# Optimization experiments

Hardware: AMD Instinct MI355X
Metric: run time of the kernel (lower is better)

The kernel has to match this reference:

```python
import jax, jax.numpy as jnp
import numpy as np

N_REAL = 1_000_000
C_IN = 32
C_OUT = 32
PAD = 1_050_000


def setup_inputs() -> dict:
    key = jax.random.key(0)
    k_x, k_fn, k_w0, k_w1, k_w2, k_b = jax.random.split(key, 6)
    x = jax.random.normal(k_x, (N_REAL, C_IN), dtype=jnp.float32)
    face_neighborhood = jax.random.randint(k_fn, (N_REAL, 9), 0, PAD, dtype=jnp.int32)
    # real faces occupy the first N_REAL padded slots; the rest are pads
    face_is_pad = jnp.arange(PAD) >= N_REAL
    # kaiming-uniform-style init for [out, in] weights (fan_in = C_IN for 1x1 taps)
    bw = 1.0 / np.sqrt(C_IN)
    w0 = jax.random.uniform(k_w0, (C_OUT, C_IN), jnp.float32, -bw, bw)
    w1 = jax.random.uniform(k_w1, (C_OUT, C_IN), jnp.float32, -bw, bw)
    w2 = jax.random.uniform(k_w2, (C_OUT, C_IN), jnp.float32, -bw, bw)
    bb = 1.0 / np.sqrt(C_IN * 9)  # fan_in of the full (out,in,1,9) kernel
    bias = jax.random.uniform(k_b, (C_OUT,), jnp.float32, -bb, bb)
    return {"x": x, "w0": w0, "w1": w1, "w2": w2, "bias": bias,
            "face_neighborhood": face_neighborhood, "face_is_pad": face_is_pad,
            "pad_size": PAD}


def reference(x, w0, w1, w2, bias, face_neighborhood, face_is_pad, pad_size):
    # Scatter x into padded buffer: padded_x[~face_is_pad] = x (jit-safe via cumsum map)
    keep = jnp.logical_not(face_is_pad)
    src = jnp.cumsum(keep.astype(jnp.int32)) - 1  # index into x for each kept slot
    padded_x = jnp.where(keep[:, None], x[jnp.clip(src, 0, x.shape[0] - 1)],
                         jnp.zeros((), x.dtype))  # [pad_size, C]
    # Symmetric 1x9 filter = [w0, w1, w2, w1, w2, w1, w2, w1, w2]:
    # fold the 9 gathers into 3 groups before the tiny GEMMs.
    g0 = padded_x[face_neighborhood[:, 0]]
    g1 = (padded_x[face_neighborhood[:, 1]] + padded_x[face_neighborhood[:, 3]]
          + padded_x[face_neighborhood[:, 5]] + padded_x[face_neighborhood[:, 7]])
    g2 = (padded_x[face_neighborhood[:, 2]] + padded_x[face_neighborhood[:, 4]]
          + padded_x[face_neighborhood[:, 6]] + padded_x[face_neighborhood[:, 8]])
    out = (jnp.einsum('nc,oc->no', g0, w0)
           + jnp.einsum('nc,oc->no', g1, w1)
           + jnp.einsum('nc,oc->no', g2, w2)
           + bias)
    return out
```

## Files before the change

### kernel.cpp

```cpp
#include <hip/hip_runtime.h>
#include <hip/hip_fp16.h>

typedef _Float16 half8 __attribute__((ext_vector_type(8)));
typedef _Float16 half4v __attribute__((ext_vector_type(4)));
typedef float float4v __attribute__((ext_vector_type(4)));
typedef int int4a __attribute__((ext_vector_type(4), aligned(4)));

#define BLOCK 256
#define ROWS_PER_BLOCK 64
#define ROWPITCH 104

__device__ _Float16 g_wh[6 * 512];

__global__ void prep_weights(const float* __restrict__ w0,
                             const float* __restrict__ w1,
                             const float* __restrict__ w2) {
    const int t = threadIdx.x;
    const int st = t >> 6;
    const int lane = t & 63;
    const int s = st >> 1, tt = st & 1;
    const float* w = (s == 0) ? w0 : (s == 1) ? w1 : w2;
    const int o = tt * 16 + (lane & 15);
    const int k = (lane >> 4) * 8;
    #pragma unroll
    for (int j = 0; j < 8; ++j)
        g_wh[st * 512 + lane * 8 + j] = (_Float16)w[o * 32 + k + j];
}

__global__ __launch_bounds__(256) void convert_x(const float* __restrict__ x,
                                                 _Float16* __restrict__ xh,
                                                 int n8) {
    const int stride = gridDim.x * 256;
    for (int i = blockIdx.x * 256 + threadIdx.x; i < n8; i += stride) {
        const float4v a = __builtin_nontemporal_load(reinterpret_cast<const float4v*>(x) + 2 * (long)i);
        const float4v b = __builtin_nontemporal_load(reinterpret_cast<const float4v*>(x) + 2 * (long)i + 1);
        half8 h = {(_Float16)a.x, (_Float16)a.y, (_Float16)a.z, (_Float16)a.w,
                   (_Float16)b.x, (_Float16)b.y, (_Float16)b.z, (_Float16)b.w};
        *(half8*)(xh + 8 * (long)i) = h;
    }
}

__global__ __launch_bounds__(BLOCK) void face_conv_f16(
    const _Float16* __restrict__ xh,
    const float* __restrict__ bias,
    const int* __restrict__ fn,
    float* __restrict__ out,
    int N)
{
    __shared__ alignas(16) _Float16 A[4][16 * ROWPITCH];

    const int tid  = threadIdx.x;
    const int wave = tid >> 6;
    const int lane = tid & 63;
    const int m16  = lane & 15;
    const int quad = lane >> 4;
    const int r    = lane >> 2;
    const int c8   = (lane & 3) * 8;

    half8 bfrag[3][2];
    #pragma unroll
    for (int s = 0; s < 3; ++s)
        #pragma unroll
        for (int t = 0; t < 2; ++t)
            bfrag[s][t] = *(const half8*)(g_wh + (s * 2 + t) * 512 + lane * 8);
    const float bias0 = bias[m16];
    const float bias1 = bias[16 + m16];

    const int base = blockIdx.x * ROWS_PER_BLOCK + wave * 16;
    _Float16* Aw = A[wave];

    int row = base + r;
    row = (row < N) ? row : (N - 1);
    const int* fr = fn + (long)row * 9;
    const int4a i03 = __builtin_nontemporal_load(reinterpret_cast<const int4a*>(fr));
    const int4a i47 = __builtin_nontemporal_load(reinterpret_cast<const int4a*>(fr + 4));
    const int  i8s  = __builtin_nontemporal_load(fr + 8);
    const int idx[9] = {i03.x, i03.y, i03.z, i03.w, i47.x, i47.y, i47.z, i47.w, i8s};

    half8 v[9];
    #pragma unroll
    for (int j = 0; j < 9; ++j) {
        const int id = idx[j];
        if ((unsigned)id < (unsigned)N) {
            v[j] = *(const half8*)(xh + (long)id * 32 + c8);
        } else {
            v[j] = (half8){0, 0, 0, 0, 0, 0, 0, 0};
        }
    }
    half8 g0 = v[0], g1, g2;
    #pragma unroll
    for (int e = 0; e < 8; ++e) {
        g1[e] = (_Float16)((float)v[1][e] + (float)v[3][e] + (float)v[5][e] + (float)v[7][e]);
        g2[e] = (_Float16)((float)v[2][e] + (float)v[4][e] + (float)v[6][e] + (float)v[8][e]);
    }
    _Float16* dst = Aw + r * ROWPITCH + c8;
    *(half8*)(dst)      = g0;
    *(half8*)(dst + 32) = g1;
    *(half8*)(dst + 64) = g2;

    __syncthreads();

    float4v acc0 = {0.f, 0.f, 0.f, 0.f}, acc1 = {0.f, 0.f, 0.f, 0.f};
    #pragma unroll
    for (int s = 0; s < 3; ++s) {
        half8 a = *(half8*)(Aw + m16 * ROWPITCH + s * 32 + quad * 8);
        acc0 = __builtin_amdgcn_mfma_f32_16x16x32_f16(a, bfrag[s][0], acc0, 0, 0, 0);
        acc1 = __builtin_amdgcn_mfma_f32_16x16x32_f16(a, bfrag[s][1], acc1, 0, 0, 0);
    }

    #pragma unroll
    for (int i = 0; i < 4; ++i) {
        const int rr = base + quad * 4 + i;
        if (rr < N) {
            __builtin_nontemporal_store(acc0[i] + bias0, &out[(long)rr * 32 + m16]);
            __builtin_nontemporal_store(acc1[i] + bias1, &out[(long)rr * 32 + 16 + m16]);
        }
    }
}

__global__ __launch_bounds__(BLOCK) void face_conv_kernel(
    const float* __restrict__ x,
    const float* __restrict__ bias,
    const int* __restrict__ fn,
    float* __restrict__ out,
    int N)
{
    __shared__ alignas(16) _Float16 A[4][16 * ROWPITCH];

    const int tid  = threadIdx.x;
    const int wave = tid >> 6;
    const int lane = tid & 63;
    const int m16  = lane & 15;
    const int quad = lane >> 4;
    const int oct  = lane >> 3;
    const int m8   = lane & 7;

    half8 bfrag[3][2];
    #pragma unroll
    for (int s = 0; s < 3; ++s)
        #pragma unroll
        for (int t = 0; t < 2; ++t)
            bfrag[s][t] = *(const half8*)(g_wh + (s * 2 + t) * 512 + lane * 8);
    const float bias0 = bias[m16];
    const float bias1 = bias[16 + m16];

    const int base = blockIdx.x * ROWS_PER_BLOCK + wave * 16;
    _Float16* Aw = A[wave];

    int idx[2][9];
    #pragma unroll
    for (int it = 0; it < 2; ++it) {
        int r = base + it * 8 + oct;
        r = (r < N) ? r : (N - 1);
        const int* fr = fn + (long)r * 9;
        #pragma unroll
        for (int j = 0; j < 9; ++j) idx[it][j] = __builtin_nontemporal_load(fr + j);
    }

    #pragma unroll
    for (int it = 0; it < 2; ++it) {
        float4v v[9];
        #pragma unroll
        for (int j = 0; j < 9; ++j) {
            const int id = idx[it][j];
            if ((unsigned)id < (unsigned)N) {
                v[j] = *(const float4v*)(x + (long)id * 32 + m8 * 4);
            } else {
                v[j] = (float4v){0.f, 0.f, 0.f, 0.f};
            }
        }
        const float4v g0 = v[0];
        const float4v g1 = v[1] + v[3] + v[5] + v[7];
        const float4v g2 = v[2] + v[4] + v[6] + v[8];
        _Float16* dst = Aw + (it * 8 + oct) * ROWPITCH + m8 * 4;
        *(half4v*)(dst)      = (half4v){(_Float16)g0.x, (_Float16)g0.y, (_Float16)g0.z, (_Float16)g0.w};
        *(half4v*)(dst + 32) = (half4v){(_Float16)g1.x, (_Float16)g1.y, (_Float16)g1.z, (_Float16)g1.w};
        *(half4v*)(dst + 64) = (half4v){(_Float16)g2.x, (_Float16)g2.y, (_Float16)g2.z, (_Float16)g2.w};
    }

    __syncthreads();

    float4v acc0 = {0.f, 0.f, 0.f, 0.f}, acc1 = {0.f, 0.f, 0.f, 0.f};
    #pragma unroll
    for (int s = 0; s < 3; ++s) {
        half8 a = *(half8*)(Aw + m16 * ROWPITCH + s * 32 + quad * 8);
        acc0 = __builtin_amdgcn_mfma_f32_16x16x32_f16(a, bfrag[s][0], acc0, 0, 0, 0);
        acc1 = __builtin_amdgcn_mfma_f32_16x16x32_f16(a, bfrag[s][1], acc1, 0, 0, 0);
    }

    #pragma unroll
    for (int i = 0; i < 4; ++i) {
        const int r = base + quad * 4 + i;
        if (r < N) {
            __builtin_nontemporal_store(acc0[i] + bias0, &out[(long)r * 32 + m16]);
            __builtin_nontemporal_store(acc1[i] + bias1, &out[(long)r * 32 + 16 + m16]);
        }
    }
}

extern "C" void kernel_launch(void* const* d_in, const int* in_sizes, int n_in,
                              void* d_out, int out_size, void* d_ws, size_t ws_size,
                              hipStream_t stream) {
    const float* x    = (const float*)d_in[0];
    const float* w0   = (const float*)d_in[1];
    const float* w1   = (const float*)d_in[2];
    const float* w2   = (const float*)d_in[3];
    const float* bias = (const float*)d_in[4];
    const int*   fn   = (const int*)d_in[5];
    float* out = (float*)d_out;

    const int N = in_sizes[0] / 32;
    const int blocks = (N + ROWS_PER_BLOCK - 1) / ROWS_PER_BLOCK;

    prep_weights<<<1, 384, 0, stream>>>(w0, w1, w2);

    const size_t need = (size_t)N * 32 * sizeof(_Float16);
    if (d_ws != nullptr && ws_size >= need) {
        _Float16* xh = (_Float16*)d_ws;
        const int n8 = N * 4;
        convert_x<<<2048, 256, 0, stream>>>(x, xh, n8);
        face_conv_f16<<<blocks, BLOCK, 0, stream>>>(xh, bias, fn, out, N);
    } else {
        face_conv_kernel<<<blocks, BLOCK, 0, stream>>>(x, bias, fn, out, N);
    }
}
```

Before: 401.6 us.

## Quantize x to per-row int8 with log-scale exponent for gather conv

Replaces the fp16 copy of x with per-row int8 values plus a one-byte scale exponent in 1/16-octave steps, so each random neighbor gather reads 8 bytes per lane instead of 16. The conv kernel dequantizes by multiplying by the per-neighbor scale, staged through shared memory, before the MFMA. Weight preparation is folded into block 0 of the quantize kernel, which removes one launch. The cost is a loss of precision, since int8 with a row-max scale is coarser than fp16, plus extra integer unpacking arithmetic and one scale-byte gather per neighbor.

```diff
diff --git a/kernel.cpp b/kernel.cpp
--- a/kernel.cpp
+++ b/kernel.cpp
@@ -5,6 +5,8 @@
 typedef _Float16 half4v __attribute__((ext_vector_type(4)));
 typedef float float4v __attribute__((ext_vector_type(4)));
 typedef int int4a __attribute__((ext_vector_type(4), aligned(4)));
+typedef int int2v __attribute__((ext_vector_type(2)));
+typedef int int4v __attribute__((ext_vector_type(4)));
 
 #define BLOCK 256
 #define ROWS_PER_BLOCK 64
@@ -12,42 +14,88 @@
 
 __device__ _Float16 g_wh[6 * 512];
 
+__device__ __forceinline__ void prep_weights_dev(const float* __restrict__ w0,
+                                                 const float* __restrict__ w1,
+                                                 const float* __restrict__ w2,
+                                                 int tid) {
+    const int lane = tid & 63;
+    for (int st = tid >> 6; st < 6; st += 4) {
+        const int s = st >> 1, tt = st & 1;
+        const float* w = (s == 0) ? w0 : (s == 1) ? w1 : w2;
+        const int o = tt * 16 + (lane & 15);
+        const int k = (lane >> 4) * 8;
+        #pragma unroll
+        for (int j = 0; j < 8; ++j)
+            g_wh[st * 512 + lane * 8 + j] = (_Float16)w[o * 32 + k + j];
+    }
+}
+
 __global__ void prep_weights(const float* __restrict__ w0,
                              const float* __restrict__ w1,
                              const float* __restrict__ w2) {
-    const int t = threadIdx.x;
-    const int st = t >> 6;
-    const int lane = t & 63;
-    const int s = st >> 1, tt = st & 1;
-    const float* w = (s == 0) ? w0 : (s == 1) ? w1 : w2;
-    const int o = tt * 16 + (lane & 15);
-    const int k = (lane >> 4) * 8;
-    #pragma unroll
-    for (int j = 0; j < 8; ++j)
-        g_wh[st * 512 + lane * 8 + j] = (_Float16)w[o * 32 + k + j];
-}
-
-__global__ __launch_bounds__(256) void convert_x(const float* __restrict__ x,
-                                                 _Float16* __restrict__ xh,
-                                                 int n8) {
+    prep_weights_dev(w0, w1, w2, (int)threadIdx.x);
+}
+
+__global__ __launch_bounds__(256) void quantize_x(const float* __restrict__ x,
+                                                  char* __restrict__ q,
+                                                  unsigned char* __restrict__ qs,
+                                                  const float* __restrict__ w0,
+                                                  const float* __restrict__ w1,
+                                                  const float* __restrict__ w2,
+                                                  int N) {
+    if (blockIdx.x == 0) prep_weights_dev(w0, w1, w2, (int)threadIdx.x);
     const int stride = gridDim.x * 256;
-    for (int i = blockIdx.x * 256 + threadIdx.x; i < n8; i += stride) {
-        const float4v a = __builtin_nontemporal_load(reinterpret_cast<const float4v*>(x) + 2 * (long)i);
-        const float4v b = __builtin_nontemporal_load(reinterpret_cast<const float4v*>(x) + 2 * (long)i + 1);
-        half8 h = {(_Float16)a.x, (_Float16)a.y, (_Float16)a.z, (_Float16)a.w,
-                   (_Float16)b.x, (_Float16)b.y, (_Float16)b.z, (_Float16)b.w};
-        *(half8*)(xh + 8 * (long)i) = h;
-    }
-}
-
-__global__ __launch_bounds__(BLOCK) void face_conv_f16(
-    const _Float16* __restrict__ xh,
+    for (int row = blockIdx.x * 256 + (int)threadIdx.x; row < N; row += stride) {
+        const float4v* xp = (const float4v*)(x + (long)row * 32);
+        float4v v[8];
+        #pragma unroll
+        for (int k = 0; k < 8; ++k) v[k] = __builtin_nontemporal_load(xp + k);
+        float m = 0.f;
+        #pragma unroll
+        for (int k = 0; k < 8; ++k)
+            m = fmaxf(m, fmaxf(fmaxf(fabsf(v[k].x), fabsf(v[k].y)),
+                               fmaxf(fabsf(v[k].z), fabsf(v[k].w))));
+        int e;
+        float inv;
+        if (m > 0.f) {
+            e = (int)ceilf(16.f * log2f(m * (1.f / 127.f)) + 0.001f);
+            e = (e < -127) ? -127 : ((e > 127) ? 127 : e);
+            inv = exp2f((float)(-e) * 0.0625f);
+        } else {
+            e = -127;
+            inv = 0.f;
+        }
+        unsigned int w[8];
+        #pragma unroll
+        for (int k = 0; k < 8; ++k) {
+            int b0 = (int)rintf(v[k].x * inv);
+            int b1 = (int)rintf(v[k].y * inv);
+            int b2 = (int)rintf(v[k].z * inv);
+            int b3 = (int)rintf(v[k].w * inv);
+            b0 = b0 > 127 ? 127 : (b0 < -127 ? -127 : b0);
+            b1 = b1 > 127 ? 127 : (b1 < -127 ? -127 : b1);
+            b2 = b2 > 127 ? 127 : (b2 < -127 ? -127 : b2);
+            b3 = b3 > 127 ? 127 : (b3 < -127 ? -127 : b3);
+            w[k] = (unsigned)(b0 & 255) | ((unsigned)(b1 & 255) << 8) |
+                   ((unsigned)(b2 & 255) << 16) | ((unsigned)(b3 & 255) << 24);
+        }
+        int4v* qp = (int4v*)(q + (long)row * 32);
+        qp[0] = (int4v){(int)w[0], (int)w[1], (int)w[2], (int)w[3]};
+        qp[1] = (int4v){(int)w[4], (int)w[5], (int)w[6], (int)w[7]};
+        qs[row] = (unsigned char)(e + 128);
+    }
+}
+
+__global__ __launch_bounds__(BLOCK) void face_conv_i8(
+    const char* __restrict__ q,
+    const unsigned char* __restrict__ qs,
     const float* __restrict__ bias,
     const int* __restrict__ fn,
     float* __restrict__ out,
     int N)
 {
     __shared__ alignas(16) _Float16 A[4][16 * ROWPITCH];
+    __shared__ float S[4][16][9];
 
     const int tid  = threadIdx.x;
     const int wave = tid >> 6;
@@ -55,7 +103,7 @@
     const int m16  = lane & 15;
     const int quad = lane >> 4;
     const int r    = lane >> 2;
-    const int c8   = (lane & 3) * 8;
+    const int c4   = lane & 3;
 
     half8 bfrag[3][2];
     #pragma unroll
@@ -77,26 +125,61 @@
     const int  i8s  = __builtin_nontemporal_load(fr + 8);
     const int idx[9] = {i03.x, i03.y, i03.z, i03.w, i47.x, i47.y, i47.z, i47.w, i8s};
 
-    half8 v[9];
+    int2v qv[9];
     #pragma unroll
     for (int j = 0; j < 9; ++j) {
         const int id = idx[j];
-        if ((unsigned)id < (unsigned)N) {
-            v[j] = *(const half8*)(xh + (long)id * 32 + c8);
-        } else {
-            v[j] = (half8){0, 0, 0, 0, 0, 0, 0, 0};
-        }
-    }
-    half8 g0 = v[0], g1, g2;
+        const int cl = ((unsigned)id < (unsigned)N) ? id : 0;
+        qv[j] = *(const int2v*)(q + ((long)cl << 5) + c4 * 8);
+    }
+
+    {
+        const int j0 = c4, j1 = c4 + 4;
+        const int id0 = idx[j0], id1 = idx[j1];
+        S[wave][r][j0] = ((unsigned)id0 < (unsigned)N)
+            ? exp2f((float)((int)qs[id0] - 128) * 0.0625f) : 0.f;
+        S[wave][r][j1] = ((unsigned)id1 < (unsigned)N)
+            ? exp2f((float)((int)qs[id1] - 128) * 0.0625f) : 0.f;
+        if (c4 == 0) {
+            const int id2 = idx[8];
+            S[wave][r][8] = ((unsigned)id2 < (unsigned)N)
+                ? exp2f((float)((int)qs[id2] - 128) * 0.0625f) : 0.f;
+        }
+    }
+    asm volatile("s_waitcnt lgkmcnt(0)" ::: "memory");
+    float sv[9];
+    #pragma unroll
+    for (int j = 0; j < 9; ++j) sv[j] = S[wave][r][j];
+
+    float g0f[8] = {0,0,0,0,0,0,0,0};
+    float g1f[8] = {0,0,0,0,0,0,0,0};
+    float g2f[8] = {0,0,0,0,0,0,0,0};
+    #pragma unroll
+    for (int j = 0; j < 9; ++j) {
+        const float s = sv[j];
+        float* g = (j == 0) ? g0f : ((j & 1) ? g1f : g2f);
+        #pragma unroll
+        for (int e = 0; e < 2; ++e) {
+            const int wrd = qv[j][e];
+            #pragma unroll
+            for (int b = 0; b < 4; ++b) {
+                const int val = (wrd << (24 - 8 * b)) >> 24;
+                g[e * 4 + b] += (float)val * s;
+            }
+        }
+    }
+
+    _Float16* dst = Aw + r * ROWPITCH + c4 * 8;
+    half8 h0, h1, h2;
     #pragma unroll
     for (int e = 0; e < 8; ++e) {
-        g1[e] = (_Float16)((float)v[1][e] + (float)v[3][e] + (float)v[5][e] + (float)v[7][e]);
-        g2[e] = (_Float16)((float)v[2][e] + (float)v[4][e] + (float)v[6][e] + (float)v[8][e]);
-    }
-    _Float16* dst = Aw + r * ROWPITCH + c8;
-    *(half8*)(dst)      = g0;
-    *(half8*)(dst + 32) = g1;
-    *(half8*)(dst + 64) = g2;
+        h0[e] = (_Float16)g0f[e];
+        h1[e] = (_Float16)g1f[e];
+        h2[e] = (_Float16)g2f[e];
+    }
+    *(half8*)(dst)      = h0;
+    *(half8*)(dst + 32) = h1;
+    *(half8*)(dst + 64) = h2;
 
     __syncthreads();
 
@@ -212,15 +295,14 @@
     const int N = in_sizes[0] / 32;
     const int blocks = (N + ROWS_PER_BLOCK - 1) / ROWS_PER_BLOCK;
 
-    prep_weights<<<1, 384, 0, stream>>>(w0, w1, w2);
-
-    const size_t need = (size_t)N * 32 * sizeof(_Float16);
+    const size_t need = (size_t)N * 32 + (size_t)N;
     if (d_ws != nullptr && ws_size >= need) {
-        _Float16* xh = (_Float16*)d_ws;
-        const int n8 = N * 4;
-        convert_x<<<2048, 256, 0, stream>>>(x, xh, n8);
-        face_conv_f16<<<blocks, BLOCK, 0, stream>>>(xh, bias, fn, out, N);
+        char* q = (char*)d_ws;
+        unsigned char* qsc = (unsigned char*)d_ws + (size_t)N * 32;
+        quantize_x<<<2048, 256, 0, stream>>>(x, q, qsc, w0, w1, w2, N);
+        face_conv_i8<<<blocks, BLOCK, 0, stream>>>(q, qsc, bias, fn, out, N);
     } else {
+        prep_weights<<<1, 384, 0, stream>>>(w0, w1, w2);
         face_conv_kernel<<<blocks, BLOCK, 0, stream>>>(x, bias, fn, out, N);
     }
 }
```

After: 426.6 us. 6.2% more time.
